# Optimization experiments

Measured on AMD Instinct MI355X. Metric: run time of the kernel, lower is better.

The kernel has to match this reference:

```python
import jax, jax.numpy as jnp
import numpy as np
from jax import lax

N = 2048
D_ENC = 64      # conv channels
D = 512         # node embedding dim (resnet18 feature dim)
K = 5           # max_num_neighbors
L_LAYERS = 4    # num_layers
ARENA = 32.0    # positions scaled to [0, ARENA)^2
R2 = 2.0        # radius^2 = (sqrt(2))^2


def setup_inputs() -> dict:
    key = jax.random.key(0)
    ks = jax.random.split(key, 9)
    imgs = jax.random.normal(ks[0], (N, 3, 64, 64), dtype=jnp.float32)
    pos = jax.random.uniform(ks[1], (N, 2), dtype=jnp.float32)  # scaled by ARENA inside
    conv_w = jax.random.normal(ks[2], (D_ENC, 3, 7, 7), dtype=jnp.float32) * 0.05
    conv_b = jnp.zeros((D_ENC,), dtype=jnp.float32)
    proj_w = jax.random.normal(ks[3], (D_ENC, D), dtype=jnp.float32) * (1.0 / np.sqrt(D_ENC))
    proj_b = jnp.zeros((D,), dtype=jnp.float32)
    w_self = jax.random.normal(ks[4], (L_LAYERS, D, D), dtype=jnp.float32) * (1.0 / np.sqrt(D))
    w_nbr = jax.random.normal(ks[5], (L_LAYERS, D, D), dtype=jnp.float32) * (1.0 / np.sqrt(D))
    b_gnn = jnp.zeros((L_LAYERS, D), dtype=jnp.float32)
    return {"imgs": imgs, "pos": pos, "conv_w": conv_w, "conv_b": conv_b,
            "proj_w": proj_w, "proj_b": proj_b,
            "w_self": w_self, "w_nbr": w_nbr, "b_gnn": b_gnn}


def _encode(imgs, conv_w, conv_b, proj_w, proj_b):
    # conv 7x7 stride 2 + relu + global avg pool + linear -> [N, D]
    x = lax.conv_general_dilated(imgs, conv_w, window_strides=(2, 2), padding="SAME",
                                 dimension_numbers=("NCHW", "OIHW", "NCHW"))
    x = jax.nn.relu(x + conv_b[None, :, None, None])
    x = x.mean(axis=(2, 3))                      # [N, D_ENC]
    return jax.nn.relu(x @ proj_w + proj_b)      # [N, D]


def _radius_knn(pos):
    # radius graph with radius sqrt(2), no self loops, capped at K neighbors
    p = pos * ARENA                              # [N, 2]
    d2 = jnp.sum((p[:, None, :] - p[None, :, :]) ** 2, axis=-1)  # [N, N]
    invalid = (d2 > R2) | jnp.eye(N, dtype=bool)
    d2m = jnp.where(invalid, jnp.inf, d2)
    neg_vals, idx = lax.top_k(-d2m, K)           # K nearest within radius
    valid = jnp.isfinite(neg_vals)               # [N, K]
    return idx, valid


def reference(imgs, pos, conv_w, conv_b, proj_w, proj_b, w_self, w_nbr, b_gnn):
    h = _encode(imgs, conv_w, conv_b, proj_w, proj_b)   # [N, D]
    idx, valid = _radius_knn(pos)                        # [N, K], [N, K]
    vmask = valid.astype(h.dtype)                        # [N, K]
    denom = jnp.maximum(vmask.sum(axis=1, keepdims=True), 1.0)  # [N, 1]
    for l in range(L_LAYERS):
        nbr = h[idx] * vmask[:, :, None]                 # [N, K, D] gather
        agg = nbr.sum(axis=1) / denom                    # mean over valid neighbors
        h = jax.nn.relu(h @ w_self[l] + agg @ w_nbr[l] + b_gnn[l])
    return h
```

## Files before the change

kernel.cpp:

```cpp
#include <hip/hip_runtime.h>


#define NNODES 2048

typedef __attribute__((ext_vector_type(8))) _Float16 half8;
typedef __attribute__((ext_vector_type(16))) float f32x16;

__global__ __launch_bounds__(256) void prep_wfrag_kernel(
    const float* __restrict__ w, ushort* __restrict__ wfrag) {
  int i = blockIdx.x * 256 + threadIdx.x;
  if (i >= 12288) return;
  int j = i & 7;
  int l = (i >> 3) & 63;
  int q = i >> 9;
  int kb = q % 12, ct = q / 12;
  int g = 2 * kb + (l >> 5);
  int c = 32 * ct + (l & 31);
  float val = 0.f;
  if (g < 21 && j < 7) val = w[c * 147 + g * 7 + j];
  wfrag[i] = __builtin_bit_cast(ushort, (_Float16)val);
}

__global__ __launch_bounds__(256) void prep_wT_kernel(
    const float* __restrict__ wsrc_s, const float* __restrict__ wsrc_n,
    ushort* __restrict__ wT) {
  __shared__ float s[64][65];
  int bid = blockIdx.x;
  int m = bid >> 6, kt = (bid >> 3) & 7, nt = bid & 7;
  const float* in = (m < 4) ? (wsrc_s + m * 262144) : (wsrc_n + (m - 4) * 262144);
  ushort* out = wT + m * 262144;
  int t = threadIdx.x;
  int k0 = kt << 6, n0 = nt << 6;
#pragma unroll
  for (int rep = 0; rep < 4; ++rep) {
    int row = (rep << 4) + (t >> 4);
    int c4 = (t & 15) << 2;
    float4 v = *(const float4*)&in[(k0 + row) * 512 + n0 + c4];
    s[row][c4] = v.x; s[row][c4 + 1] = v.y; s[row][c4 + 2] = v.z; s[row][c4 + 3] = v.w;
  }
  __syncthreads();
#pragma unroll
  for (int rep = 0; rep < 4; ++rep) {
    int n = (rep << 4) + (t >> 4);
    int k4 = (t & 15) << 2;
    ushort4 o;
    o.x = __builtin_bit_cast(ushort, (_Float16)s[k4 + 0][n]);
    o.y = __builtin_bit_cast(ushort, (_Float16)s[k4 + 1][n]);
    o.z = __builtin_bit_cast(ushort, (_Float16)s[k4 + 2][n]);
    o.w = __builtin_bit_cast(ushort, (_Float16)s[k4 + 3][n]);
    *(ushort4*)&out[(n0 + n) * 512 + k0 + k4] = o;
  }
}

__device__ inline uint pack2h(float x, float y) {
  ushort a = __builtin_bit_cast(ushort, (_Float16)x);
  ushort b = __builtin_bit_cast(ushort, (_Float16)y);
  return (uint)a | ((uint)b << 16);
}

__global__ __launch_bounds__(256) void conv_pool_kernel(
    const float* __restrict__ imgs, const ushort* __restrict__ wfrag,
    const float* __restrict__ cb, float* __restrict__ enc) {
  __shared__ ushort s_img[14904];
  __shared__ float s_pool[64];
  const int n = blockIdx.x;
  const int tid = threadIdx.x;
  const int lane = tid & 63;
  const int w = tid >> 6;
  const int hi = lane >> 5;
  const int lo = lane & 31;

  half8 bf[24];
  const half8* wf = (const half8*)wfrag;
#pragma unroll
  for (int q = 0; q < 24; ++q) bf[q] = wf[q * 64 + lane];

  int4 z = {0, 0, 0, 0};
  for (int i = tid; i < 1863; i += 256) ((int4*)s_img)[i] = z;
  if (tid < 64) s_pool[tid] = 0.f;
  __syncthreads();

  const float4* src = (const float4*)(imgs + (size_t)n * 12288);
  for (int i = tid; i < 3072; i += 256) {
    float4 v = src[i];
    int e = i << 2;
    int c = e >> 12;
    int rem = e & 4095;
    int y = rem >> 6, x = rem & 63;
    int d = (c * 69 + y + 2) * 72 + x + 2;
    ((uint*)s_img)[d >> 1] = pack2h(v.x, v.y);
    ((uint*)s_img)[(d >> 1) + 1] = pack2h(v.z, v.w);
  }

  int aoff[12];
#pragma unroll
  for (int kb = 0; kb < 12; ++kb) {
    int g = 2 * kb + hi;
    if (g > 20) g = 20;
    int ic = g / 7, ky = g - ic * 7;
    aoff[kb] = (ic * 69 + ky) * 144 + 4 * lo + w * 2304;
  }
  const float bias0 = cb[lo];
  const float bias1 = cb[32 + lo];
  float pool0 = 0.f, pool1 = 0.f;
  __syncthreads();

  const char* sb = (const char*)s_img;
  for (int tp = 0; tp < 4; ++tp) {
    f32x16 a0 = {}, a1 = {}, a2 = {}, a3 = {};
#pragma unroll
    for (int kb = 0; kb < 12; ++kb) {
      const char* p = sb + aoff[kb] + tp * 576;
      union { half8 v; uint u[4]; } f0, f1;
      f0.u[0] = *(const uint*)(p);
      f0.u[1] = *(const uint*)(p + 4);
      f0.u[2] = *(const uint*)(p + 8);
      f0.u[3] = *(const uint*)(p + 12);
      f1.u[0] = *(const uint*)(p + 288);
      f1.u[1] = *(const uint*)(p + 292);
      f1.u[2] = *(const uint*)(p + 296);
      f1.u[3] = *(const uint*)(p + 300);
      a0 = __builtin_amdgcn_mfma_f32_32x32x16_f16(f0.v, bf[kb],      a0, 0, 0, 0);
      a1 = __builtin_amdgcn_mfma_f32_32x32x16_f16(f0.v, bf[12 + kb], a1, 0, 0, 0);
      a2 = __builtin_amdgcn_mfma_f32_32x32x16_f16(f1.v, bf[kb],      a2, 0, 0, 0);
      a3 = __builtin_amdgcn_mfma_f32_32x32x16_f16(f1.v, bf[12 + kb], a3, 0, 0, 0);
    }
    float s0 = 0.f, s1 = 0.f;
#pragma unroll
    for (int r = 0; r < 16; ++r) {
      s0 += fmaxf(a0[r] + bias0, 0.f) + fmaxf(a2[r] + bias0, 0.f);
      s1 += fmaxf(a1[r] + bias1, 0.f) + fmaxf(a3[r] + bias1, 0.f);
    }
    pool0 += s0;
    pool1 += s1;
  }
  pool0 += __shfl_xor(pool0, 32);
  pool1 += __shfl_xor(pool1, 32);
  if (lane < 32) {
    atomicAdd(&s_pool[lo], pool0);
    atomicAdd(&s_pool[32 + lo], pool1);
  }
  __syncthreads();
  if (tid < 64) enc[n * 64 + tid] = s_pool[tid] * (1.f / 1024.f);
}

__global__ __launch_bounds__(256) void proj_kernel(
    const float* __restrict__ enc, const float* __restrict__ pw,
    const float* __restrict__ pb, ushort* __restrict__ h16) {
  int c = ((blockIdx.x & 1) << 8) | threadIdx.x;
  int r0 = (blockIdx.x >> 1) << 3;
  float bias = pb[c];
  float acc[8];
#pragma unroll
  for (int r = 0; r < 8; ++r) acc[r] = bias;
#pragma unroll 4
  for (int k = 0; k < 64; ++k) {
    float w = pw[k * 512 + c];
#pragma unroll
    for (int r = 0; r < 8; ++r) acc[r] = fmaf(enc[(r0 + r) * 64 + k], w, acc[r]);
  }
#pragma unroll
  for (int r = 0; r < 8; ++r)
    h16[(r0 + r) * 512 + c] = __builtin_bit_cast(ushort, (_Float16)fmaxf(acc[r], 0.f));
}

__global__ __launch_bounds__(256) void knn_kernel(
    const float* __restrict__ pos, int* __restrict__ nbr, float* __restrict__ den) {
  __shared__ float s_d2[NNODES];
  __shared__ int s_idx[NNODES];
  __shared__ int s_cnt;
  const int i = blockIdx.x;
  const int tid = threadIdx.x;
  if (tid == 0) s_cnt = 0;
  __syncthreads();
  const float px = pos[2 * i] * 32.f, py = pos[2 * i + 1] * 32.f;
#pragma unroll
  for (int r = 0; r < 8; ++r) {
    int j = tid + (r << 8);
    float2 q = ((const float2*)pos)[j];
    float dx = q.x * 32.f - px, dy = q.y * 32.f - py;
    float d2 = dx * dx + dy * dy;
    if (d2 <= 2.0f && j != i) {
      int slot = atomicAdd(&s_cnt, 1);
      s_d2[slot] = d2;
      s_idx[slot] = j;
    }
  }
  __syncthreads();
  if (tid < 64) {
    const int lane = tid;
    const int cnt = s_cnt;
    int nf = 0;
#pragma unroll
    for (int k = 0; k < 5; ++k) {
      float best = 1e30f;
      int bslot = 0x7fffffff;
      for (int e = lane; e < cnt; e += 64) {
        float d = s_d2[e];
        if (d < best) { best = d; bslot = e; }
      }
#pragma unroll
      for (int off = 1; off < 64; off <<= 1) {
        float od = __shfl_xor(best, off);
        int os = __shfl_xor(bslot, off);
        if (od < best || (od == best && os < bslot)) { best = od; bslot = os; }
      }
      bool got = (best < 1e30f);
      if (lane == 0) nbr[i * 5 + k] = got ? s_idx[bslot] : -1;
      if (got) { s_d2[bslot] = 1e30f; ++nf; }
    }
    if (lane == 0) den[i] = 1.f / (float)(nf > 0 ? nf : 1);
  }
}

__global__ __launch_bounds__(256) void agg_kernel(
    const ushort* __restrict__ h16, const int* __restrict__ nbr,
    const float* __restrict__ den, ushort* __restrict__ agg16) {
  int i = blockIdx.x >> 1;
  int d = ((blockIdx.x & 1) << 8) + threadIdx.x;
  const _Float16* hp = (const _Float16*)h16;
  float s = 0.f;
#pragma unroll
  for (int k = 0; k < 5; ++k) {
    int j = nbr[i * 5 + k];
    if (j >= 0) s += (float)hp[j * 512 + d];
  }
  agg16[i * 512 + d] = __builtin_bit_cast(ushort, (_Float16)(s * den[i]));
}

__global__ __launch_bounds__(256) void gnn_gemm_kernel(
    const ushort* __restrict__ hA, const ushort* __restrict__ agg,
    const ushort* __restrict__ Ws, const ushort* __restrict__ Wn,
    const float* __restrict__ bias, ushort* __restrict__ hout,
    float* __restrict__ fout, int final_layer) {
  __shared__ ushort s_lds[2][16384];
  const int tid = threadIdx.x;
  const int lane = tid & 63;
  const int hi = lane >> 5, lo = lane & 31;
  const int wu = __builtin_amdgcn_readfirstlane(tid >> 6);
  const int wr = wu >> 1, wc = wu & 1;
  const int bm = blockIdx.x >> 3, bn = blockIdx.x & 7;
  const int r0 = bm << 6, c0 = bn << 6;

  auto STAGE = [&](int buf, int it) {
    int k0 = it << 6;
    const ushort* ph = hA  + (r0 + lane) * 512 + k0 + 8 * wu;
    const ushort* pg = agg + (r0 + lane) * 512 + k0 + 8 * wu;
    const ushort* ps = Ws  + (c0 + lane) * 512 + k0 + 8 * wu;
    const ushort* pn = Wn  + (c0 + lane) * 512 + k0 + 8 * wu;
    ushort* lb = &s_lds[buf][wu << 9];
#define GLDS(SRC, DST) __builtin_amdgcn_global_load_lds( \
      (const __attribute__((address_space(1))) void*)(SRC), \
      (__attribute__((address_space(3))) void*)(DST), 16, 0, 0)
    GLDS(ph, lb);            GLDS(ph + 32, lb + 2048);
    GLDS(pg, lb + 4096);     GLDS(pg + 32, lb + 6144);
    GLDS(ps, lb + 8192);     GLDS(ps + 32, lb + 10240);
    GLDS(pn, lb + 12288);    GLDS(pn + 32, lb + 14336);
#undef GLDS
  };

  f32x16 accS = {}, accN = {};
  STAGE(0, 0);
  __syncthreads();
  int cur = 0;
  for (int it = 0; it < 8; ++it) {
    if (it < 7) STAGE(cur ^ 1, it + 1);
    const half8* pAh = (const half8*)&s_lds[cur][0];
    const half8* pAg = (const half8*)&s_lds[cur][4096];
    const half8* pBs = (const half8*)&s_lds[cur][8192];
    const half8* pBn = (const half8*)&s_lds[cur][12288];
#pragma unroll
    for (int ks = 0; ks < 4; ++ks) {
      int gi = (2 * ks + hi) * 64;
      half8 ah = pAh[gi + 32 * wr + lo];
      half8 bs = pBs[gi + 32 * wc + lo];
      accS = __builtin_amdgcn_mfma_f32_32x32x16_f16(ah, bs, accS, 0, 0, 0);
      half8 ag = pAg[gi + 32 * wr + lo];
      half8 bn2 = pBn[gi + 32 * wc + lo];
      accN = __builtin_amdgcn_mfma_f32_32x32x16_f16(ag, bn2, accN, 0, 0, 0);
    }
    __syncthreads();
    cur ^= 1;
  }

  const int col = c0 + 32 * wc + lo;
  const float b = bias[col];
#pragma unroll
  for (int r = 0; r < 16; ++r) {
    int row = r0 + 32 * wr + (r & 3) + ((r >> 2) << 3) + (hi << 2);
    float v = fmaxf(accS[r] + accN[r] + b, 0.f);
    if (final_layer) fout[row * 512 + col] = v;
    else hout[row * 512 + col] = __builtin_bit_cast(ushort, (_Float16)v);
  }
}

extern "C" void kernel_launch(void* const* d_in, const int* in_sizes, int n_in,
                              void* d_out, int out_size, void* d_ws, size_t ws_size,
                              hipStream_t stream) {
  const float* imgs   = (const float*)d_in[0];
  const float* pos    = (const float*)d_in[1];
  const float* conv_w = (const float*)d_in[2];
  const float* conv_b = (const float*)d_in[3];
  const float* proj_w = (const float*)d_in[4];
  const float* proj_b = (const float*)d_in[5];
  const float* w_self = (const float*)d_in[6];
  const float* w_nbr  = (const float*)d_in[7];
  const float* b_gnn  = (const float*)d_in[8];

  char* ws = (char*)d_ws;
  ushort* wfrag = (ushort*)(ws);
  float*  enc   = (float*) (ws + 32768);
  ushort* h16a  = (ushort*)(ws + 557056);
  ushort* h16b  = (ushort*)(ws + 2654208);
  ushort* agg16 = (ushort*)(ws + 4751360);
  ushort* wT16  = (ushort*)(ws + 6848512);
  int*    nbr   = (int*)   (ws + 11042816);
  float*  den   = (float*) (ws + 11083776);

  prep_wfrag_kernel<<<48, 256, 0, stream>>>(conv_w, wfrag);
  prep_wT_kernel<<<512, 256, 0, stream>>>(w_self, w_nbr, wT16);
  knn_kernel<<<NNODES, 256, 0, stream>>>(pos, nbr, den);
  conv_pool_kernel<<<NNODES, 256, 0, stream>>>(imgs, wfrag, conv_b, enc);
  proj_kernel<<<512, 256, 0, stream>>>(enc, proj_w, proj_b, h16a);

  for (int l = 0; l < 4; ++l) {
    ushort* hin  = (l & 1) ? h16b : h16a;
    ushort* hnew = (l & 1) ? h16a : h16b;
    agg_kernel<<<4096, 256, 0, stream>>>(hin, nbr, den, agg16);
    gnn_gemm_kernel<<<256, 256, 0, stream>>>(
        hin, agg16, wT16 + l * 262144, wT16 + (4 + l) * 262144,
        b_gnn + l * 512, hnew, (float*)d_out, (l == 3) ? 1 : 0);
  }
}
```

Baseline: 160.3 us.

## Split conv_pool per image into two half-row blocks with LDS weights and prefetch

Splits each image's conv+pool across two blocks, each handling 32 output rows with a halo-sized LDS tile, so the grid doubles and per-block LDS shrinks. Conv weight fragments move from 24 register half8s into LDS, and the kernel gets occupancy hint 3 to lower register pressure. The K loop is software-pipelined with a two-stage fragment prefetch. Partial pools are combined by a global atomicAdd into enc, which is zeroed with a memset beforehand. This adds extra launches, LDS weight reads and nondeterministic float summation order.

```diff
diff --git a/kernel.cpp b/kernel.cpp
--- a/kernel.cpp
+++ b/kernel.cpp
@@ -58,38 +58,44 @@
   return (uint)a | ((uint)b << 16);
 }
 
-__global__ __launch_bounds__(256) void conv_pool_kernel(
+__global__ __launch_bounds__(256, 3) void conv_pool_kernel(
     const float* __restrict__ imgs, const ushort* __restrict__ wfrag,
     const float* __restrict__ cb, float* __restrict__ enc) {
-  __shared__ ushort s_img[14904];
-  __shared__ float s_pool[64];
-  const int n = blockIdx.x;
+  __shared__ int4 s_all[2599];
+  ushort* s_img = (ushort*)s_all;
+  const half8* swf8 = (const half8*)((char*)s_all + 15984);
+  float* s_pool = (float*)((char*)s_all + 40560);
+
+  const int n = blockIdx.x >> 1;
+  const int r0half = blockIdx.x & 1;
+  const int wy = 32 * r0half - 2;
   const int tid = threadIdx.x;
   const int lane = tid & 63;
   const int w = tid >> 6;
   const int hi = lane >> 5;
   const int lo = lane & 31;
 
-  half8 bf[24];
-  const half8* wf = (const half8*)wfrag;
-#pragma unroll
-  for (int q = 0; q < 24; ++q) bf[q] = wf[q * 64 + lane];
-
   int4 z = {0, 0, 0, 0};
-  for (int i = tid; i < 1863; i += 256) ((int4*)s_img)[i] = z;
-  if (tid < 64) s_pool[tid] = 0.f;
-  __syncthreads();
+  for (int i = tid; i < 999; i += 256) s_all[i] = z;
+  __syncthreads();
+
+  const int4* wf4 = (const int4*)wfrag;
+  int4* swf4 = (int4*)((char*)s_all + 15984);
+#pragma unroll
+  for (int r = 0; r < 6; ++r) swf4[tid + r * 256] = wf4[tid + r * 256];
 
   const float4* src = (const float4*)(imgs + (size_t)n * 12288);
-  for (int i = tid; i < 3072; i += 256) {
-    float4 v = src[i];
-    int e = i << 2;
-    int c = e >> 12;
-    int rem = e & 4095;
-    int y = rem >> 6, x = rem & 63;
-    int d = (c * 69 + y + 2) * 72 + x + 2;
-    ((uint*)s_img)[d >> 1] = pack2h(v.x, v.y);
-    ((uint*)s_img)[(d >> 1) + 1] = pack2h(v.z, v.w);
+  for (int i = tid; i < 1776; i += 256) {
+    int ic = i / 592;
+    int rem = i - ic * 592;
+    int li = rem >> 4, xq = rem & 15;
+    int iy = wy + li;
+    if (iy >= 0 && iy < 64) {
+      float4 v = src[(ic * 64 + iy) * 16 + xq];
+      int d = (ic * 37 + li) * 72 + (xq << 2) + 2;
+      ((uint*)s_img)[d >> 1] = pack2h(v.x, v.y);
+      ((uint*)s_img)[(d >> 1) + 1] = pack2h(v.z, v.w);
+    }
   }
 
   int aoff[12];
@@ -98,7 +104,7 @@
     int g = 2 * kb + hi;
     if (g > 20) g = 20;
     int ic = g / 7, ky = g - ic * 7;
-    aoff[kb] = (ic * 69 + ky) * 144 + 4 * lo + w * 2304;
+    aoff[kb] = (ic * 37 + ky) * 144 + 4 * lo + w * 1152;
   }
   const float bias0 = cb[lo];
   const float bias1 = cb[32 + lo];
@@ -106,24 +112,36 @@
   __syncthreads();
 
   const char* sb = (const char*)s_img;
-  for (int tp = 0; tp < 4; ++tp) {
+  union F { half8 v; uint u[4]; };
+
+#define LOADF(F0, F1, B0, B1, KB, TPADD) do {                       \
+    const char* p_ = sb + aoff[KB] + (TPADD);                       \
+    F0.u[0] = *(const uint*)(p_);       F0.u[1] = *(const uint*)(p_ + 4);   \
+    F0.u[2] = *(const uint*)(p_ + 8);   F0.u[3] = *(const uint*)(p_ + 12);  \
+    F1.u[0] = *(const uint*)(p_ + 288); F1.u[1] = *(const uint*)(p_ + 292); \
+    F1.u[2] = *(const uint*)(p_ + 296); F1.u[3] = *(const uint*)(p_ + 300); \
+    B0 = swf8[(KB) * 64 + lane];        B1 = swf8[(12 + (KB)) * 64 + lane]; \
+  } while (0)
+
+#pragma unroll
+  for (int tp = 0; tp < 2; ++tp) {
+    const int tpadd = tp * 576;
     f32x16 a0 = {}, a1 = {}, a2 = {}, a3 = {};
-#pragma unroll
-    for (int kb = 0; kb < 12; ++kb) {
-      const char* p = sb + aoff[kb] + tp * 576;
-      union { half8 v; uint u[4]; } f0, f1;
-      f0.u[0] = *(const uint*)(p);
-      f0.u[1] = *(const uint*)(p + 4);
-      f0.u[2] = *(const uint*)(p + 8);
-      f0.u[3] = *(const uint*)(p + 12);
-      f1.u[0] = *(const uint*)(p + 288);
-      f1.u[1] = *(const uint*)(p + 292);
-      f1.u[2] = *(const uint*)(p + 296);
-      f1.u[3] = *(const uint*)(p + 300);
-      a0 = __builtin_amdgcn_mfma_f32_32x32x16_f16(f0.v, bf[kb],      a0, 0, 0, 0);
-      a1 = __builtin_amdgcn_mfma_f32_32x32x16_f16(f0.v, bf[12 + kb], a1, 0, 0, 0);
-      a2 = __builtin_amdgcn_mfma_f32_32x32x16_f16(f1.v, bf[kb],      a2, 0, 0, 0);
-      a3 = __builtin_amdgcn_mfma_f32_32x32x16_f16(f1.v, bf[12 + kb], a3, 0, 0, 0);
+    F f0a, f1a, f0b, f1b;
+    half8 b0a, b1a, b0b, b1b;
+    LOADF(f0a, f1a, b0a, b1a, 0, tpadd);
+#pragma unroll
+    for (int kb = 0; kb < 12; kb += 2) {
+      LOADF(f0b, f1b, b0b, b1b, kb + 1, tpadd);
+      a0 = __builtin_amdgcn_mfma_f32_32x32x16_f16(f0a.v, b0a, a0, 0, 0, 0);
+      a1 = __builtin_amdgcn_mfma_f32_32x32x16_f16(f0a.v, b1a, a1, 0, 0, 0);
+      a2 = __builtin_amdgcn_mfma_f32_32x32x16_f16(f1a.v, b0a, a2, 0, 0, 0);
+      a3 = __builtin_amdgcn_mfma_f32_32x32x16_f16(f1a.v, b1a, a3, 0, 0, 0);
+      if (kb + 2 < 12) LOADF(f0a, f1a, b0a, b1a, kb + 2, tpadd);
+      a0 = __builtin_amdgcn_mfma_f32_32x32x16_f16(f0b.v, b0b, a0, 0, 0, 0);
+      a1 = __builtin_amdgcn_mfma_f32_32x32x16_f16(f0b.v, b1b, a1, 0, 0, 0);
+      a2 = __builtin_amdgcn_mfma_f32_32x32x16_f16(f1b.v, b0b, a2, 0, 0, 0);
+      a3 = __builtin_amdgcn_mfma_f32_32x32x16_f16(f1b.v, b1b, a3, 0, 0, 0);
     }
     float s0 = 0.f, s1 = 0.f;
 #pragma unroll
@@ -134,14 +152,19 @@
     pool0 += s0;
     pool1 += s1;
   }
+#undef LOADF
+
   pool0 += __shfl_xor(pool0, 32);
   pool1 += __shfl_xor(pool1, 32);
   if (lane < 32) {
-    atomicAdd(&s_pool[lo], pool0);
-    atomicAdd(&s_pool[32 + lo], pool1);
-  }
-  __syncthreads();
-  if (tid < 64) enc[n * 64 + tid] = s_pool[tid] * (1.f / 1024.f);
+    s_pool[w * 64 + lo] = pool0;
+    s_pool[w * 64 + 32 + lo] = pool1;
+  }
+  __syncthreads();
+  if (tid < 64) {
+    float s = s_pool[tid] + s_pool[64 + tid] + s_pool[128 + tid] + s_pool[192 + tid];
+    atomicAdd(&enc[n * 64 + tid], s * (1.f / 1024.f));
+  }
 }
 
 __global__ __launch_bounds__(256) void proj_kernel(
@@ -320,7 +343,8 @@
   prep_wfrag_kernel<<<48, 256, 0, stream>>>(conv_w, wfrag);
   prep_wT_kernel<<<512, 256, 0, stream>>>(w_self, w_nbr, wT16);
   knn_kernel<<<NNODES, 256, 0, stream>>>(pos, nbr, den);
-  conv_pool_kernel<<<NNODES, 256, 0, stream>>>(imgs, wfrag, conv_b, enc);
+  hipMemsetAsync(enc, 0, 524288, stream);
+  conv_pool_kernel<<<2 * NNODES, 256, 0, stream>>>(imgs, wfrag, conv_b, enc);
   proj_kernel<<<512, 256, 0, stream>>>(enc, proj_w, proj_b, h16a);
 
   for (int l = 0; l < 4; ++l) {
```

New measurement: 161.0 us. Within noise of the previous version (+0.5%).
